# Kernel optimization log

Measured on AMD Instinct MI355X. Metric: run time of the kernel, lower is better.

The kernel has to match this reference:

```python
import jax, jax.numpy as jnp
import numpy as np

HORIZON = 1024
N_EMBD = 256
N_LAYER = 4
ACTION_DIM = 10
DIM = 64
ACT_NUM = 10
N_POS = 4 * (1 + HORIZON)
FEAT = 3 + DIM * ACT_NUM + ACTION_DIM  # 653
EPS = 1e-5
BATCH = 8


def _layernorm(x, g, b):
    m = jnp.mean(x, axis=-1, keepdims=True)
    v = jnp.mean((x - m) ** 2, axis=-1, keepdims=True)
    return (x - m) * jax.lax.rsqrt(v + EPS) * g + b


def setup_inputs() -> dict:
    key = jax.random.key(0)
    ks = jax.random.split(key, 16)
    f = jnp.float32
    L, E = N_LAYER, N_EMBD
    return {
        'query_states': jax.random.normal(ks[0], (BATCH, 64), f),
        'action_set': jax.random.normal(ks[1], (BATCH, ACT_NUM, DIM), f),
        'context_actions': jax.random.normal(ks[2], (BATCH, HORIZON, ACTION_DIM), f),
        'context_rewards': jax.random.normal(ks[3], (BATCH, HORIZON, 1), f),
        'W_embed': jax.random.normal(ks[4], (FEAT, E), f) * 0.02,
        'b_embed': jnp.zeros((E,), f),
        'wpe': jax.random.normal(ks[5], (N_POS, E), f) * 0.02,
        'Wq': jax.random.normal(ks[6], (L, E, E), f) * 0.02,
        'Wk': jax.random.normal(ks[7], (L, E, E), f) * 0.02,
        'Wv': jax.random.normal(ks[8], (L, E, E), f) * 0.02,
        'ln1_g': jnp.ones((L, E), f),
        'ln1_b': jnp.zeros((L, E), f),
        'W1': jax.random.normal(ks[9], (L, E, E), f) * 0.02,
        'b1': jnp.zeros((L, E), f),
        'W2': jax.random.normal(ks[10], (L, E, E), f) * 0.02,
        'b2': jnp.zeros((L, E), f),
        'ln2_g': jnp.ones((L, E), f),
        'ln2_b': jnp.zeros((L, E), f),
        'W_pred': jax.random.normal(ks[11], (E, ACTION_DIM), f) * 0.02,
        'b_pred': jnp.zeros((ACTION_DIM,), f),
    }


def reference(query_states, action_set, context_actions, context_rewards,
              W_embed, b_embed, wpe, Wq, Wk, Wv,
              ln1_g, ln1_b, W1, b1, W2, b2, ln2_g, ln2_b,
              W_pred, b_pred):
    B = action_set.shape[0]
    T = context_actions.shape[1]
    A = context_actions.shape[2]
    N = 2 * T
    # --- build the interleaved sequence (test=False path) ---
    aset0 = action_set.reshape(B, 1, -1)                         # [B,1,dim*act_num]
    aset = jnp.concatenate([aset0, jnp.zeros_like(aset0)], axis=1)  # [B,2,F0]
    aset = jnp.tile(aset, (1, T, 1))                              # [B,2T,F0]
    action_seq = jnp.zeros((B, N, A + 1), dtype=context_actions.dtype)
    action_seq = action_seq.at[:, 1::2, :].set(
        jnp.concatenate([context_actions, context_rewards], axis=2))
    one_seq = jnp.ones((B, N, 1), dtype=context_actions.dtype)
    pos_seq = jnp.broadcast_to(
        jnp.arange(1, N + 1, dtype=context_actions.dtype).reshape(1, N, 1), (B, N, 1))
    seq = jnp.concatenate([aset, action_seq, one_seq, pos_seq], axis=2)  # [B,N,FEAT]
    # --- embed + positional embedding ---
    H = seq @ W_embed + b_embed          # [B,N,E]
    H = H + wpe[:N]                       # position_ids = arange(N)
    # --- causal mask with per-row 1/(i+1) normalization ---
    i = jnp.arange(N)[:, None]
    j = jnp.arange(N)[None, :]
    mask = jnp.where(j <= i, 1.0 / (i + 1).astype(H.dtype), 0.0)  # [N,N]
    # --- decoder layers: relu(QK^T)*mask attention + MLP, layernorms ---
    for l in range(N_LAYER):
        q = H @ Wq[l]
        k = H @ Wk[l]
        v = H @ Wv[l]
        attn = jax.nn.relu(jnp.einsum('bid,bjd->bij', q, k)) * mask  # [B,N,N]
        H = H + jnp.einsum('bij,bjd->bid', attn, v)
        H = _layernorm(H, ln1_g[l], ln1_b[l])
        H = H + jax.nn.relu(H @ W1[l] + b1[l]) @ W2[l] + b2[l]
        H = _layernorm(H, ln2_g[l], ln2_b[l])
    preds = H @ W_pred + b_pred           # [B,N,action_dim]
    return preds[:, 0::2, :]              # [B,T,action_dim]
```

## Files before the change

### kernel.cpp

```cpp
#include <hip/hip_runtime.h>


#define BB 8
#define TT 1024
#define NN 2048
#define EE 256
#define LL 4

typedef __attribute__((ext_vector_type(8))) short short8;
typedef __attribute__((ext_vector_type(4))) float f32x4;

__device__ inline ushort f2b(float f) {
    union { float f; unsigned u; } x; x.f = f;
    unsigned u = x.u;
    return (ushort)((u + 0x7fffu + ((u >> 16) & 1u)) >> 16);
}
__device__ inline unsigned cvtpk(float lo, float hi) {
    unsigned r;
    asm volatile("v_cvt_pk_bf16_f32 %0, %1, %2" : "=v"(r) : "v"(lo), "v"(hi));
    return r;
}
__device__ inline size_t pk256(int row, int k) {
    return ((size_t)((row >> 4) * 8 + (k >> 5))) * 512
         + (size_t)((((k >> 3) & 3) * 16 + (row & 15)) * 8 + (k & 7));
}
__device__ inline size_t vpk_idx(int bb, int nn, int e) {
    return ((size_t)(bb*64 + (nn >> 5)) * 16 + (e >> 4)) * 512
         + (size_t)((((nn >> 3) & 3) * 16 + (e & 15)) * 8 + (nn & 7));
}

__global__ __launch_bounds__(256) void wprep_k(
    const float* __restrict__ Wq, const float* __restrict__ Wk,
    const float* __restrict__ Wv, const float* __restrict__ W1,
    const float* __restrict__ W2,
    ushort* __restrict__ WQKt, ushort* __restrict__ WVt,
    ushort* __restrict__ W1t, ushort* __restrict__ W2t)
{
    int id = blockIdx.x;
    int m = id >> 4, t = id & 15;
    int l = m / 5, which = m % 5;
    const float* src; ushort* dst;
    size_t o = (size_t)l * 65536;
    switch (which) {
        case 0: src = Wq + o; dst = WQKt + (size_t)l*131072;          break;
        case 1: src = Wk + o; dst = WQKt + (size_t)l*131072 + 65536;  break;
        case 2: src = Wv + o; dst = WVt + o; break;
        case 3: src = W1 + o; dst = W1t + o; break;
        default: src = W2 + o; dst = W2t + o; break;
    }
    int tk = (t >> 2) * 64;
    int tn = (t & 3) * 64;
    __shared__ ushort T[64][68];
    int tid = threadIdx.x;
    int r = tid >> 4, c4 = (tid & 15) * 4;
    #pragma unroll
    for (int it = 0; it < 4; ++it) {
        int k = r + it*16;
        float4 v = *(const float4*)&src[(size_t)(tk + k)*256 + tn + c4];
        T[k][c4+0] = f2b(v.x); T[k][c4+1] = f2b(v.y);
        T[k][c4+2] = f2b(v.z); T[k][c4+3] = f2b(v.w);
    }
    __syncthreads();
    #pragma unroll
    for (int it = 0; it < 4; ++it) {
        int n = tn + r + it*16;
        int k0 = tk + c4;
        ushort4 ov;
        ov.x = T[c4+0][n-tn]; ov.y = T[c4+1][n-tn];
        ov.z = T[c4+2][n-tn]; ov.w = T[c4+3][n-tn];
        *(ushort4*)&dst[pk256(n, k0)] = ov;
    }
}

__global__ __launch_bounds__(256) void base_even_k(
    const float* __restrict__ aset, const float* __restrict__ We,
    const float* __restrict__ be, float* __restrict__ BE)
{
    int b = blockIdx.x; int e = threadIdx.x;
    __shared__ float as[640];
    for (int i = e; i < 640; i += 256) as[i] = aset[b*640 + i];
    __syncthreads();
    float s = We[651*EE + e] + be[e];
    for (int f = 0; f < 640; ++f) s = fmaf(as[f], We[f*EE + e], s);
    BE[b*EE + e] = s;
}

__global__ __launch_bounds__(256) void embed_k(
    const float* __restrict__ BE, const float* __restrict__ ca,
    const float* __restrict__ cr, const float* __restrict__ We,
    const float* __restrict__ be, const float* __restrict__ wpe,
    float* __restrict__ H, ushort* __restrict__ Hbf)
{
    int e = threadIdx.x;
    #pragma unroll
    for (int k = 0; k < 8; ++k) {
        int rb = blockIdx.x * 8 + k;
        int b = rb >> 11, n = rb & (NN-1);
        float h;
        if ((n & 1) == 0) {
            h = BE[b*EE + e];
        } else {
            int t = n >> 1;
            h = We[651*EE + e] + be[e];
            const float* cap = ca + (size_t)(b*TT + t)*10;
            #pragma unroll
            for (int i = 0; i < 10; ++i) h = fmaf(cap[i], We[(640+i)*EE + e], h);
            h = fmaf(cr[b*TT + t], We[650*EE + e], h);
        }
        h = fmaf((float)(n + 1), We[652*EE + e], h);
        h += wpe[(size_t)n*EE + e];
        H[(size_t)rb*EE + e] = h;
        Hbf[pk256(rb, e)] = f2b(h);
    }
}

__global__ __launch_bounds__(256, 2) void qkv_k(
    const ushort* __restrict__ A, const ushort* __restrict__ WQK,
    const ushort* __restrict__ WV,
    ushort* __restrict__ Qo, ushort* __restrict__ Ko, ushort* __restrict__ Vo)
{
    int tid = threadIdx.x;
    int w = tid >> 6, l = tid & 63;
    int lr = l & 15, lg = l >> 4;
    int wr = w >> 1, wc = w & 1;
    int rt0 = blockIdx.x * 8 + wr*4;
    int ct0 = blockIdx.y * 8 + wc*4;
    const ushort* Ap = A + (size_t)rt0*4096 + l*8;
    const ushort* Bp = (blockIdx.y < 4 ? WQK + (size_t)ct0*4096
                                       : WV + (size_t)(ct0-32)*4096) + l*8;
    f32x4 acc[4][4];
    #pragma unroll
    for (int i = 0; i < 4; ++i)
        #pragma unroll
        for (int j = 0; j < 4; ++j) acc[i][j] = (f32x4){0.f,0.f,0.f,0.f};
    #pragma unroll
    for (int kc = 0; kc < 8; ++kc) {
        short8 af[4], bf[4];
        #pragma unroll
        for (int rg = 0; rg < 4; ++rg) af[rg] = *(const short8*)(Ap + (size_t)rg*4096 + kc*512);
        #pragma unroll
        for (int cg = 0; cg < 4; ++cg) bf[cg] = *(const short8*)(Bp + (size_t)cg*4096 + kc*512);
        #pragma unroll
        for (int rg = 0; rg < 4; ++rg)
            #pragma unroll
            for (int cg = 0; cg < 4; ++cg)
                acc[rg][cg] = __builtin_amdgcn_mfma_f32_16x16x32_bf16(af[rg], bf[cg], acc[rg][cg], 0,0,0);
    }
    #pragma unroll
    for (int rg = 0; rg < 4; ++rg)
        #pragma unroll
        for (int cg = 0; cg < 4; ++cg)
            #pragma unroll
            for (int r = 0; r < 4; ++r) {
                int row = rt0*16 + rg*16 + lg*4 + r;
                int col = ct0*16 + cg*16 + lr;
                ushort xv = f2b(acc[rg][cg][r]);
                if (col < 256)      Qo[pk256(row, col)] = xv;
                else if (col < 512) Ko[pk256(row, col - 256)] = xv;
                else {
                    int e = col - 512, bb = row >> 11, nn = row & (NN-1);
                    Vo[vpk_idx(bb, nn, e)] = xv;
                }
            }
}

__global__ __launch_bounds__(256, 2) void mlp1_k(
    const ushort* __restrict__ A, const ushort* __restrict__ Bw,
    const float* __restrict__ bias, ushort* __restrict__ Cv)
{
    int tid = threadIdx.x;
    int w = tid >> 6, l = tid & 63;
    int lr = l & 15, lg = l >> 4;
    int wr = w >> 1, wc = w & 1;
    int rt0 = blockIdx.x * 8 + wr*4;
    int ct0 = blockIdx.y * 8 + wc*4;
    const ushort* Ap = A  + (size_t)rt0*4096 + l*8;
    const ushort* Bp = Bw + (size_t)ct0*4096 + l*8;
    f32x4 acc[4][4];
    #pragma unroll
    for (int i = 0; i < 4; ++i)
        #pragma unroll
        for (int j = 0; j < 4; ++j) acc[i][j] = (f32x4){0.f,0.f,0.f,0.f};
    #pragma unroll
    for (int kc = 0; kc < 8; ++kc) {
        short8 af[4], bf[4];
        #pragma unroll
        for (int rg = 0; rg < 4; ++rg) af[rg] = *(const short8*)(Ap + (size_t)rg*4096 + kc*512);
        #pragma unroll
        for (int cg = 0; cg < 4; ++cg) bf[cg] = *(const short8*)(Bp + (size_t)cg*4096 + kc*512);
        #pragma unroll
        for (int rg = 0; rg < 4; ++rg)
            #pragma unroll
            for (int cg = 0; cg < 4; ++cg)
                acc[rg][cg] = __builtin_amdgcn_mfma_f32_16x16x32_bf16(af[rg], bf[cg], acc[rg][cg], 0,0,0);
    }
    #pragma unroll
    for (int rg = 0; rg < 4; ++rg)
        #pragma unroll
        for (int cg = 0; cg < 4; ++cg)
            #pragma unroll
            for (int r = 0; r < 4; ++r) {
                int row = rt0*16 + rg*16 + lg*4 + r;
                int col = ct0*16 + cg*16 + lr;
                float x = fmaxf(acc[rg][cg][r] + bias[col], 0.f);
                Cv[pk256(row, col)] = f2b(x);
            }
}

__global__ __launch_bounds__(256, 2) void mlp2ln_k(
    const ushort* __restrict__ A, const ushort* __restrict__ Bw,
    const float* __restrict__ bias, const float* __restrict__ Res,
    const float* __restrict__ g, const float* __restrict__ bt,
    float* __restrict__ Hout, ushort* __restrict__ Hpk)
{
    int tid = threadIdx.x;
    int w = tid >> 6, l = tid & 63;
    int lr = l & 15, lg = l >> 4;
    int rt0 = blockIdx.x * 2;
    int ct0 = w * 4;
    const ushort* Ap = A  + (size_t)rt0*4096 + l*8;
    const ushort* Bp = Bw + (size_t)ct0*4096 + l*8;
    f32x4 acc[2][4];
    #pragma unroll
    for (int i = 0; i < 2; ++i)
        #pragma unroll
        for (int j = 0; j < 4; ++j) acc[i][j] = (f32x4){0.f,0.f,0.f,0.f};
    #pragma unroll
    for (int kc = 0; kc < 8; ++kc) {
        short8 a0 = *(const short8*)(Ap + kc*512);
        short8 a1 = *(const short8*)(Ap + 4096 + kc*512);
        short8 bf[4];
        #pragma unroll
        for (int cg = 0; cg < 4; ++cg) bf[cg] = *(const short8*)(Bp + (size_t)cg*4096 + kc*512);
        #pragma unroll
        for (int cg = 0; cg < 4; ++cg) {
            acc[0][cg] = __builtin_amdgcn_mfma_f32_16x16x32_bf16(a0, bf[cg], acc[0][cg], 0,0,0);
            acc[1][cg] = __builtin_amdgcn_mfma_f32_16x16x32_bf16(a1, bf[cg], acc[1][cg], 0,0,0);
        }
    }
    __shared__ float red[32][4][2];
    float sm[2][4] = {}, sq[2][4] = {};
    #pragma unroll
    for (int rg = 0; rg < 2; ++rg)
        #pragma unroll
        for (int cg = 0; cg < 4; ++cg)
            #pragma unroll
            for (int r = 0; r < 4; ++r) {
                int grow = blockIdx.x*32 + rg*16 + lg*4 + r;
                int col = w*64 + cg*16 + lr;
                float v = acc[rg][cg][r] + bias[col] + Res[(size_t)grow*EE + col];
                acc[rg][cg][r] = v;
                sm[rg][r] += v; sq[rg][r] += v*v;
            }
    #pragma unroll
    for (int off = 1; off < 16; off <<= 1)
        #pragma unroll
        for (int rg = 0; rg < 2; ++rg)
            #pragma unroll
            for (int r = 0; r < 4; ++r) {
                sm[rg][r] += __shfl_xor(sm[rg][r], off);
                sq[rg][r] += __shfl_xor(sq[rg][r], off);
            }
    if (lr == 0) {
        #pragma unroll
        for (int rg = 0; rg < 2; ++rg)
            #pragma unroll
            for (int r = 0; r < 4; ++r) {
                int rl = rg*16 + lg*4 + r;
                red[rl][w][0] = sm[rg][r];
                red[rl][w][1] = sq[rg][r];
            }
    }
    __syncthreads();
    #pragma unroll
    for (int rg = 0; rg < 2; ++rg)
        #pragma unroll
        for (int r = 0; r < 4; ++r) {
            int rl = rg*16 + lg*4 + r;
            float S  = red[rl][0][0] + red[rl][1][0] + red[rl][2][0] + red[rl][3][0];
            float S2 = red[rl][0][1] + red[rl][1][1] + red[rl][2][1] + red[rl][3][1];
            float mean = S * (1.0f/256.0f);
            float var  = S2 * (1.0f/256.0f) - mean*mean;
            float inv  = 1.0f / sqrtf(var + 1e-5f);
            int grow = blockIdx.x*32 + rl;
            #pragma unroll
            for (int cg = 0; cg < 4; ++cg) {
                int col = w*64 + cg*16 + lr;
                float y = (acc[rg][cg][r] - mean) * inv * g[col] + bt[col];
                Hout[(size_t)grow*EE + col] = y;
                Hpk[pk256(grow, col)] = f2b(y);
            }
        }
}

__global__ __launch_bounds__(512, 2) void attn_k(
    const ushort* __restrict__ Qp, const ushort* __restrict__ Kp,
    const ushort* __restrict__ Vp, const float* __restrict__ H,
    const float* __restrict__ g, const float* __restrict__ bt,
    float* __restrict__ Xout, ushort* __restrict__ Lpk)
{
    int blk = blockIdx.x;
    int pk = blk >> 3, b = blk & 7;
    int tid = threadIdx.x;
    int w = tid >> 6, l = tid & 63;
    int lr = l & 15, lg = l >> 4;
    int sel  = (w & 1) ^ ((w >> 2) & 1);
    int part = w >> 1;
    int s  = sel ? (127 - pk) : pk;
    int i0 = s * 16;
    int NT = (s >> 1) + 1;
    int j0 = (part * NT) >> 2;
    int j1 = ((part + 1) * NT) >> 2;

    __shared__ float comb[2][5440];

    const ushort* Qt    = Qp + (size_t)(b*128 + s) * 4096 + l*8;
    const ushort* Kbase = Kp + (size_t)(b*128) * 4096 + l*8;
    const ushort* Vbase = Vp + (size_t)(b*64) * 16 * 512 + l*8;

    short8 qb[8];
    #pragma unroll
    for (int kc = 0; kc < 8; ++kc) qb[kc] = *(const short8*)(Qt + kc*512);

    f32x4 oacc[16];
    #pragma unroll
    for (int et = 0; et < 16; ++et) oacc[et] = (f32x4){0.f,0.f,0.f,0.f};

    int ig = i0 + lr;
    for (int jt = j0; jt < j1; ++jt) {
        const ushort* Kt = Kbase + (size_t)(jt*2) * 4096;
        short8 ka0[8], ka1[8];
        #pragma unroll
        for (int kc = 0; kc < 8; ++kc) {
            ka0[kc] = *(const short8*)(Kt + kc*512);
            ka1[kc] = *(const short8*)(Kt + 4096 + kc*512);
        }
        const ushort* Vt = Vbase + (size_t)(jt*16) * 512;
        short8 vf[16];
        #pragma unroll
        for (int et = 0; et < 16; ++et)
            vf[et] = *(const short8*)(Vt + et*512);
        f32x4 c0a = {0.f,0.f,0.f,0.f}, c0b = {0.f,0.f,0.f,0.f};
        f32x4 c1a = {0.f,0.f,0.f,0.f}, c1b = {0.f,0.f,0.f,0.f};
        #pragma unroll
        for (int kc = 0; kc < 8; kc += 2) {
            c0a = __builtin_amdgcn_mfma_f32_16x16x32_bf16(ka0[kc],   qb[kc],   c0a, 0,0,0);
            c0b = __builtin_amdgcn_mfma_f32_16x16x32_bf16(ka0[kc+1], qb[kc+1], c0b, 0,0,0);
            c1a = __builtin_amdgcn_mfma_f32_16x16x32_bf16(ka1[kc],   qb[kc],   c1a, 0,0,0);
            c1b = __builtin_amdgcn_mfma_f32_16x16x32_bf16(ka1[kc+1], qb[kc+1], c1b, 0,0,0);
        }
        f32x4 c0 = c0a + c0b, c1 = c1a + c1b;
        #pragma unroll
        for (int r = 0; r < 4; ++r) {
            int jg = jt*32 + lg*4 + r;
            c0[r] = (jg <= ig) ? fmaxf(c0[r], 0.f) : 0.f;
            c1[r] = (jg + 16 <= ig) ? fmaxf(c1[r], 0.f) : 0.f;
        }
        unsigned u0 = cvtpk(c0[0], c0[1]), u1 = cvtpk(c0[2], c0[3]);
        unsigned u2 = cvtpk(c1[0], c1[1]), u3 = cvtpk(c1[2], c1[3]);
        int srcA = 32*(lg & 1) + lr;
        int srcB = srcA + 16;
        unsigned a0A = __shfl((int)u0, srcA), a1A = __shfl((int)u1, srcA);
        unsigned a0B = __shfl((int)u0, srcB), a1B = __shfl((int)u1, srcB);
        unsigned b0A = __shfl((int)u2, srcA), b1A = __shfl((int)u3, srcA);
        unsigned b0B = __shfl((int)u2, srcB), b1B = __shfl((int)u3, srcB);
        bool lo = (lg < 2);
        union { unsigned u[4]; short8 v; } sv;
        sv.u[0] = lo ? a0A : b0A;
        sv.u[1] = lo ? a1A : b1A;
        sv.u[2] = lo ? a0B : b0B;
        sv.u[3] = lo ? a1B : b1B;
        short8 sa = sv.v;
        __builtin_amdgcn_s_setprio(1);
        #pragma unroll
        for (int et = 0; et < 16; ++et)
            oacc[et] = __builtin_amdgcn_mfma_f32_16x16x32_bf16(sa, vf[et], oacc[et], 0,0,0);
        __builtin_amdgcn_s_setprio(0);
    }

    float* cb = &comb[sel][0];
    #pragma unroll
    for (int rnd = 1; rnd <= 3; ++rnd) {
        if (part == rnd) {
            #pragma unroll
            for (int et = 0; et < 16; ++et)
                #pragma unroll
                for (int r = 0; r < 4; ++r) {
                    int idx = et*340 + l*5 + r;
                    float v = oacc[et][r];
                    if (rnd == 1) cb[idx] = v; else cb[idx] += v;
                }
        }
        __syncthreads();
    }
    if (part == 0) {
        float sm[4] = {0.f,0.f,0.f,0.f}, sq[4] = {0.f,0.f,0.f,0.f};
        #pragma unroll
        for (int et = 0; et < 16; ++et)
            #pragma unroll
            for (int r = 0; r < 4; ++r) {
                int irow = i0 + lg*4 + r;
                size_t base = ((size_t)(b*NN + irow))*EE + et*16 + lr;
                float x = H[base] + (oacc[et][r] + cb[et*340 + l*5 + r])
                                    * (1.0f / (float)(irow + 1));
                oacc[et][r] = x;
                sm[r] += x; sq[r] += x*x;
            }
        #pragma unroll
        for (int off = 1; off < 16; off <<= 1)
            #pragma unroll
            for (int r = 0; r < 4; ++r) {
                sm[r] += __shfl_xor(sm[r], off);
                sq[r] += __shfl_xor(sq[r], off);
            }
        float mean[4], inv[4];
        #pragma unroll
        for (int r = 0; r < 4; ++r) {
            mean[r] = sm[r] * (1.0f/256.0f);
            float var = sq[r] * (1.0f/256.0f) - mean[r]*mean[r];
            inv[r] = 1.0f / sqrtf(var + 1e-5f);
        }
        #pragma unroll
        for (int et = 0; et < 16; ++et) {
            int col = et*16 + lr;
            float gv = g[col], bv = bt[col];
            #pragma unroll
            for (int r = 0; r < 4; ++r) {
                int irow = i0 + lg*4 + r;
                size_t base = ((size_t)(b*NN + irow))*EE + col;
                float y = (oacc[et][r] - mean[r]) * inv[r] * gv + bv;
                Xout[base] = y;
                Lpk[pk256(b*NN + irow, col)] = f2b(y);
            }
        }
    }
}

__global__ __launch_bounds__(256) void pred_k(
    const float* __restrict__ H, const float* __restrict__ Wp,
    const float* __restrict__ bp, float* __restrict__ out)
{
    int bt = blockIdx.x;
    int b = bt >> 10, t = bt & 1023;
    size_t row = (size_t)b*NN + 2*t;
    __shared__ float hs[256];
    __shared__ float pr[16][16];
    int tid = threadIdx.x;
    hs[tid] = H[row*EE + tid];
    __syncthreads();
    int c = tid & 15, seg = tid >> 4;
    float p = 0.f;
    if (c < 10) {
        #pragma unroll
        for (int e2 = 0; e2 < 16; ++e2)
            p = fmaf(hs[seg*16 + e2], Wp[(seg*16 + e2)*10 + c], p);
    }
    pr[seg][c] = p;
    __syncthreads();
    if (tid < 10) {
        float sacc = bp[tid];
        #pragma unroll
        for (int k2 = 0; k2 < 16; ++k2) sacc += pr[k2][tid];
        out[(size_t)bt*10 + tid] = sacc;
    }
}

extern "C" void kernel_launch(void* const* d_in, const int* in_sizes, int n_in,
                              void* d_out, int out_size, void* d_ws, size_t ws_size,
                              hipStream_t stream)
{
    const float* action_set = (const float*)d_in[1];
    const float* ctx_act    = (const float*)d_in[2];
    const float* ctx_rew    = (const float*)d_in[3];
    const float* W_embed    = (const float*)d_in[4];
    const float* b_embed    = (const float*)d_in[5];
    const float* wpe        = (const float*)d_in[6];
    const float* Wq         = (const float*)d_in[7];
    const float* Wk         = (const float*)d_in[8];
    const float* Wv         = (const float*)d_in[9];
    const float* ln1g       = (const float*)d_in[10];
    const float* ln1b       = (const float*)d_in[11];
    const float* W1         = (const float*)d_in[12];
    const float* b1         = (const float*)d_in[13];
    const float* W2         = (const float*)d_in[14];
    const float* b2         = (const float*)d_in[15];
    const float* ln2g       = (const float*)d_in[16];
    const float* ln2b       = (const float*)d_in[17];
    const float* Wp         = (const float*)d_in[18];
    const float* bp         = (const float*)d_in[19];
    float* out = (float*)d_out;

    float* ws = (float*)d_ws;
    const size_t SZ = (size_t)BB*NN*EE;
    size_t o = 0;
    float*  Hb   = ws;               o += SZ;
    float*  Xb   = ws + o;           o += SZ;
    ushort* Hbf  = (ushort*)(ws+o);  o += SZ/2;
    ushort* Qp   = (ushort*)(ws+o);  o += SZ/2;
    ushort* Kpk  = (ushort*)(ws+o);  o += SZ/2;
    ushort* Vpk  = (ushort*)(ws+o);  o += SZ/2;
    ushort* WQKt = (ushort*)(ws+o);  o += 262144;
    ushort* WVt  = (ushort*)(ws+o);  o += 131072;
    ushort* W1t  = (ushort*)(ws+o);  o += 131072;
    ushort* W2t  = (ushort*)(ws+o);  o += 131072;
    float*  BE   = ws + o;

    wprep_k<<<320, 256, 0, stream>>>(Wq, Wk, Wv, W1, W2, WQKt, WVt, W1t, W2t);
    base_even_k<<<BB, 256, 0, stream>>>(action_set, W_embed, b_embed, BE);
    embed_k<<<BB*NN/8, 256, 0, stream>>>(BE, ctx_act, ctx_rew, W_embed, b_embed, wpe, Hb, Hbf);

    for (int l = 0; l < LL; ++l) {
        qkv_k<<<dim3(128, 6), 256, 0, stream>>>(
            Hbf, WQKt + (size_t)l*131072, WVt + (size_t)l*65536, Qp, Kpk, Vpk);
        attn_k<<<512, 512, 0, stream>>>(
            Qp, Kpk, Vpk, Hb, ln1g + l*EE, ln1b + l*EE, Xb, Hbf);
        mlp1_k<<<dim3(128, 2), 256, 0, stream>>>(
            Hbf, W1t + (size_t)l*65536, b1 + l*EE, Qp);
        mlp2ln_k<<<512, 256, 0, stream>>>(
            Qp, W2t + (size_t)l*65536, b2 + l*EE, Xb,
            ln2g + l*EE, ln2b + l*EE, Hb, Hbf);
    }
    pred_k<<<BB*TT, 256, 0, stream>>>(Hb, Wp, bp, out);
}
```

Measured before the change: 446.3 us.

## Fuse first MLP GEMM into attention epilogue via LDS-staged activations

Removes the separate mlp1 kernel. After the attention+layernorm epilogue, each attention block now stages its bf16 normalized 16-row tiles in shared memory and computes the ReLU(x·W1+b1) GEMM for those rows itself, with each wave covering 64 output columns. The result is written into the Q buffer, which is safe because each block reads only its own Q tiles. This saves one launch per layer plus the global write and re-read of the packed post-LN activations. In exchange it adds about 16KB of LDS per block and a serialized GEMM tail in the already long attention kernel.

New measurement: 419.6 us. -6.0%, faster.

```diff
diff --git a/kernel.cpp b/kernel.cpp
--- a/kernel.cpp
+++ b/kernel.cpp
@@ -164,49 +164,6 @@
             }
 }
 
-__global__ __launch_bounds__(256, 2) void mlp1_k(
-    const ushort* __restrict__ A, const ushort* __restrict__ Bw,
-    const float* __restrict__ bias, ushort* __restrict__ Cv)
-{
-    int tid = threadIdx.x;
-    int w = tid >> 6, l = tid & 63;
-    int lr = l & 15, lg = l >> 4;
-    int wr = w >> 1, wc = w & 1;
-    int rt0 = blockIdx.x * 8 + wr*4;
-    int ct0 = blockIdx.y * 8 + wc*4;
-    const ushort* Ap = A  + (size_t)rt0*4096 + l*8;
-    const ushort* Bp = Bw + (size_t)ct0*4096 + l*8;
-    f32x4 acc[4][4];
-    #pragma unroll
-    for (int i = 0; i < 4; ++i)
-        #pragma unroll
-        for (int j = 0; j < 4; ++j) acc[i][j] = (f32x4){0.f,0.f,0.f,0.f};
-    #pragma unroll
-    for (int kc = 0; kc < 8; ++kc) {
-        short8 af[4], bf[4];
-        #pragma unroll
-        for (int rg = 0; rg < 4; ++rg) af[rg] = *(const short8*)(Ap + (size_t)rg*4096 + kc*512);
-        #pragma unroll
-        for (int cg = 0; cg < 4; ++cg) bf[cg] = *(const short8*)(Bp + (size_t)cg*4096 + kc*512);
-        #pragma unroll
-        for (int rg = 0; rg < 4; ++rg)
-            #pragma unroll
-            for (int cg = 0; cg < 4; ++cg)
-                acc[rg][cg] = __builtin_amdgcn_mfma_f32_16x16x32_bf16(af[rg], bf[cg], acc[rg][cg], 0,0,0);
-    }
-    #pragma unroll
-    for (int rg = 0; rg < 4; ++rg)
-        #pragma unroll
-        for (int cg = 0; cg < 4; ++cg)
-            #pragma unroll
-            for (int r = 0; r < 4; ++r) {
-                int row = rt0*16 + rg*16 + lg*4 + r;
-                int col = ct0*16 + cg*16 + lr;
-                float x = fmaxf(acc[rg][cg][r] + bias[col], 0.f);
-                Cv[pk256(row, col)] = f2b(x);
-            }
-}
-
 __global__ __launch_bounds__(256, 2) void mlp2ln_k(
     const ushort* __restrict__ A, const ushort* __restrict__ Bw,
     const float* __restrict__ bias, const float* __restrict__ Res,
@@ -294,10 +251,11 @@
 }
 
 __global__ __launch_bounds__(512, 2) void attn_k(
-    const ushort* __restrict__ Qp, const ushort* __restrict__ Kp,
+    const ushort* Qp, const ushort* __restrict__ Kp,
     const ushort* __restrict__ Vp, const float* __restrict__ H,
     const float* __restrict__ g, const float* __restrict__ bt,
-    float* __restrict__ Xout, ushort* __restrict__ Lpk)
+    const ushort* __restrict__ W1t, const float* __restrict__ b1p,
+    float* __restrict__ Xout, ushort* Mid)
 {
     int blk = blockIdx.x;
     int pk = blk >> 3, b = blk & 7;
@@ -313,8 +271,9 @@
     int j1 = ((part + 1) * NT) >> 2;
 
     __shared__ float comb[2][5440];
-
-    const ushort* Qt    = Qp + (size_t)(b*128 + s) * 4096 + l*8;
+    __shared__ ushort ylds[2][4096];
+
+    const ushort* Qt    = Qp + ((size_t)(b*128 + s)) * 4096 + l*8;
     const ushort* Kbase = Kp + (size_t)(b*128) * 4096 + l*8;
     const ushort* Vbase = Vp + (size_t)(b*64) * 16 * 512 + l*8;
 
@@ -420,6 +379,7 @@
             float var = sq[r] * (1.0f/256.0f) - mean[r]*mean[r];
             inv[r] = 1.0f / sqrtf(var + 1e-5f);
         }
+        ushort* yl = &ylds[sel][0];
         #pragma unroll
         for (int et = 0; et < 16; ++et) {
             int col = et*16 + lr;
@@ -430,9 +390,37 @@
                 size_t base = ((size_t)(b*NN + irow))*EE + col;
                 float y = (oacc[et][r] - mean[r]) * inv[r] * gv + bv;
                 Xout[base] = y;
-                Lpk[pk256(b*NN + irow, col)] = f2b(y);
-            }
-        }
+                int idx = (col >> 5)*512 + ((((col >> 3) & 3) << 4) + lg*4 + r)*8
+                        + (col & 7);
+                yl[idx] = f2b(y);
+            }
+        }
+    }
+    __syncthreads();
+    {
+        const ushort* Ay = &ylds[sel][0] + l*8;
+        const ushort* Bp = W1t + (size_t)(part*4)*4096 + l*8;
+        f32x4 macc[4];
+        #pragma unroll
+        for (int cg = 0; cg < 4; ++cg) macc[cg] = (f32x4){0.f,0.f,0.f,0.f};
+        #pragma unroll
+        for (int kc = 0; kc < 8; ++kc) {
+            short8 af = *(const short8*)(Ay + kc*512);
+            #pragma unroll
+            for (int cg = 0; cg < 4; ++cg) {
+                short8 bf = *(const short8*)(Bp + (size_t)cg*4096 + kc*512);
+                macc[cg] = __builtin_amdgcn_mfma_f32_16x16x32_bf16(af, bf, macc[cg], 0,0,0);
+            }
+        }
+        #pragma unroll
+        for (int cg = 0; cg < 4; ++cg)
+            #pragma unroll
+            for (int r = 0; r < 4; ++r) {
+                int row = i0 + lg*4 + r;
+                int col = part*64 + cg*16 + lr;
+                float x = fmaxf(macc[cg][r] + b1p[col], 0.f);
+                Mid[pk256(b*NN + row, col)] = f2b(x);
+            }
     }
 }
 
@@ -513,9 +501,8 @@
         qkv_k<<<dim3(128, 6), 256, 0, stream>>>(
             Hbf, WQKt + (size_t)l*131072, WVt + (size_t)l*65536, Qp, Kpk, Vpk);
         attn_k<<<512, 512, 0, stream>>>(
-            Qp, Kpk, Vpk, Hb, ln1g + l*EE, ln1b + l*EE, Xb, Hbf);
-        mlp1_k<<<dim3(128, 2), 256, 0, stream>>>(
-            Hbf, W1t + (size_t)l*65536, b1 + l*EE, Qp);
+            Qp, Kpk, Vpk, Hb, ln1g + l*EE, ln1b + l*EE,
+            W1t + (size_t)l*65536, b1 + l*EE, Xb, Qp);
         mlp2ln_k<<<512, 256, 0, stream>>>(
             Qp, W2t + (size_t)l*65536, b2 + l*EE, Xb,
             ln2g + l*EE, ln2b + l*EE, Hb, Hbf);
```
